# Optimization experiments

Measured on AMD Instinct MI355X. Metric: run time of the kernel, lower is better.

## Reference

```python
import jax, jax.numpy as jnp
import numpy as np

VOCAB = 32000
EMB = 256
DEC = 1024
ENC = 1024  # 2 * encoder hidden (bi-directional)
B = 128
S = 512


def setup_inputs() -> dict:
    key = jax.random.key(0)
    ks = jax.random.split(key, 16)
    s = 0.02
    return {
        "inputs": jax.random.randint(ks[0], (B, 1), 0, VOCAB),
        "decoder_hidden": jax.random.normal(ks[1], (B, DEC), jnp.float32),
        "encoder_output": jax.random.normal(ks[2], (B, S, ENC), jnp.float32),
        "emb": jax.random.normal(ks[3], (VOCAB, EMB), jnp.float32) * s,
        "W1": jax.random.normal(ks[4], (ENC, DEC), jnp.float32) * s,
        "b1": jnp.zeros((DEC,), jnp.float32),
        "W2": jax.random.normal(ks[5], (DEC, DEC), jnp.float32) * s,
        "b2": jnp.zeros((DEC,), jnp.float32),
        "Wv": jax.random.normal(ks[6], (DEC, 1), jnp.float32) * s,
        "bv": jnp.zeros((1,), jnp.float32),
        "lstm_k": jax.random.normal(ks[7], (ENC + EMB, 4 * DEC), jnp.float32) * s,
        "lstm_rk": jax.random.normal(ks[8], (DEC, 4 * DEC), jnp.float32) * s,
        "lstm_b": jnp.zeros((4 * DEC,), jnp.float32),
        "fc_W": jax.random.normal(ks[9], (DEC, VOCAB), jnp.float32) * s,
        "fc_b": jnp.zeros((VOCAB,), jnp.float32),
    }


def reference(inputs, decoder_hidden, encoder_output, emb, W1, b1, W2, b2,
              Wv, bv, lstm_k, lstm_rk, lstm_b, fc_W, fc_b):
    # Bahdanau additive attention
    # score: (B, S, 1)
    hidden_proj = decoder_hidden @ W2 + b2                      # (B, DEC)
    score = jnp.tanh(encoder_output @ W1 + b1 + hidden_proj[:, None, :]) @ Wv + bv
    attention_weights = jax.nn.softmax(score, axis=1)           # (B, S, 1)
    context = jnp.sum(attention_weights * encoder_output, axis=1)  # (B, ENC)

    # embedding lookup of the single input token, concat [context, embed]
    x = jnp.concatenate([context, emb[inputs[:, 0]]], axis=-1)  # (B, ENC+EMB)

    # single-step LSTM. Original calls rnn(inputs) with NO initial_state,
    # so h0 = c0 = 0 and the recurrent kernel contributes nothing this step.
    z = x @ lstm_k + lstm_b + jnp.zeros((B, DEC), x.dtype) @ lstm_rk  # (B, 4*DEC)
    i, f, g, o = jnp.split(z, 4, axis=-1)  # keras gate order i,f,c,o
    c = jax.nn.sigmoid(f) * 0.0 + jax.nn.sigmoid(i) * jnp.tanh(g)
    h = jax.nn.sigmoid(o) * jnp.tanh(c)

    logits = h @ fc_W + fc_b                                    # (B, VOCAB)
    return logits, (h, c), attention_weights
```

## Files before the change

kernel.cpp:

```cpp
#include <hip/hip_runtime.h>
#include <hip/hip_bf16.h>

#define VOCAB 32000
#define EMB   256
#define DEC   1024
#define ENC   1024
#define BB    128
#define SS    512
#define MTOT  (BB * SS)
#define XCOLS (ENC + EMB)
#define NG    (4 * DEC)

typedef _Float16 half8  __attribute__((ext_vector_type(8)));
typedef _Float16 half4  __attribute__((ext_vector_type(4)));
typedef float    floatx4 __attribute__((ext_vector_type(4)));

__device__ __forceinline__ float fast_tanh(float x) {
    float e = __builtin_amdgcn_exp2f(x * 2.885390082f);
    return 1.0f - 2.0f * __builtin_amdgcn_rcpf(e + 1.0f);
}
__device__ __forceinline__ float fast_sigmoid(float x) {
    float e = __builtin_amdgcn_exp2f(-x * 1.442695041f);
    return __builtin_amdgcn_rcpf(1.0f + e);
}

__global__ void k_transpose_w1(const float* __restrict__ W1, _Float16* __restrict__ w1t) {
    __shared__ float tile[32][33];
    const int k0 = blockIdx.y * 32, n0 = blockIdx.x * 32;
    const int tx = threadIdx.x, ty = threadIdx.y;
    #pragma unroll
    for (int j = 0; j < 4; ++j)
        tile[ty + j * 8][tx] = W1[(size_t)(k0 + ty + j * 8) * DEC + n0 + tx];
    __syncthreads();
    #pragma unroll
    for (int j = 0; j < 4; ++j)
        w1t[(size_t)(n0 + ty + j * 8) * ENC + k0 + tx] = (_Float16)tile[tx][ty + j * 8];
}

__global__ void k_hidden_proj(const float* __restrict__ dh, const float* __restrict__ W2,
                              const float* __restrict__ b1, const float* __restrict__ b2,
                              float* __restrict__ hp) {
    __shared__ float xs[8 * 1024];
    const int t = threadIdx.x;
    const int n = blockIdx.x * 128 + t;
    const int b0 = blockIdx.y * 8;
    for (int i = t; i < 2048; i += 128)
        ((floatx4*)xs)[i] = ((const floatx4*)(dh + (size_t)b0 * 1024))[i];
    __syncthreads();
    float acc[8] = {0, 0, 0, 0, 0, 0, 0, 0};
    for (int k = 0; k < 1024; ++k) {
        float wval = W2[(size_t)k * 1024 + n];
        #pragma unroll
        for (int j = 0; j < 8; ++j) acc[j] += xs[j * 1024 + k] * wval;
    }
    const float bias = b1[n] + b2[n];
    #pragma unroll
    for (int j = 0; j < 8; ++j) hp[(size_t)(b0 + j) * 1024 + n] = acc[j] + bias;
}

__global__ __launch_bounds__(256) void k_score(
    const float* __restrict__ enc, const _Float16* __restrict__ w1t,
    const float* __restrict__ hp, const float* __restrict__ wv,
    float* __restrict__ scores)
{
    __shared__ _Float16 As[128 * 40];
    __shared__ _Float16 Bs[128 * 40];
    const int n0 = blockIdx.x * 128;
    const int m0 = blockIdx.y * 128;
    const int b  = m0 >> 9;
    const int t = threadIdx.x;
    const int lane = t & 63, w = t >> 6;
    const int wm = (w >> 1) * 64, wn = (w & 1) * 64;
    const int col = lane & 15, q = lane >> 4;

    floatx4 acc[4][4];
    #pragma unroll
    for (int i = 0; i < 4; ++i)
        #pragma unroll
        for (int j = 0; j < 4; ++j) acc[i][j] = (floatx4){0.f, 0.f, 0.f, 0.f};

    const int sr = t >> 1;
    const int sc = (t & 1) * 16;
    const float*    ag = enc + (size_t)(m0 + sr) * ENC + sc;
    const _Float16* bg = w1t + (size_t)(n0 + sr) * ENC + sc;
    _Float16* asw = &As[sr * 40 + sc];
    _Float16* bsw = &Bs[sr * 40 + sc];

    for (int k0 = 0; k0 < ENC; k0 += 32) {
        __syncthreads();
        floatx4 a0 = *(const floatx4*)(ag + k0);
        floatx4 a1 = *(const floatx4*)(ag + k0 + 4);
        floatx4 a2 = *(const floatx4*)(ag + k0 + 8);
        floatx4 a3 = *(const floatx4*)(ag + k0 + 12);
        half8 bv0 = *(const half8*)(bg + k0);
        half8 bv1 = *(const half8*)(bg + k0 + 8);
        half8 ha, hb;
        #pragma unroll
        for (int e = 0; e < 4; ++e) { ha[e] = (_Float16)a0[e]; ha[e + 4] = (_Float16)a1[e]; }
        #pragma unroll
        for (int e = 0; e < 4; ++e) { hb[e] = (_Float16)a2[e]; hb[e + 4] = (_Float16)a3[e]; }
        *(half8*)(asw)     = ha;
        *(half8*)(asw + 8) = hb;
        *(half8*)(bsw)     = bv0;
        *(half8*)(bsw + 8) = bv1;
        __syncthreads();
        half8 af[4], bf[4];
        #pragma unroll
        for (int i = 0; i < 4; ++i)
            af[i] = *(const half8*)(&As[(wm + i * 16 + col) * 40 + q * 8]);
        #pragma unroll
        for (int j = 0; j < 4; ++j)
            bf[j] = *(const half8*)(&Bs[(wn + j * 16 + col) * 40 + q * 8]);
        #pragma unroll
        for (int i = 0; i < 4; ++i)
            #pragma unroll
            for (int j = 0; j < 4; ++j)
                acc[i][j] = __builtin_amdgcn_mfma_f32_16x16x32_f16(af[i], bf[j], acc[i][j], 0, 0, 0);
    }

    float hpv[4], wvv[4];
    #pragma unroll
    for (int j = 0; j < 4; ++j) {
        int n = n0 + wn + j * 16 + col;
        hpv[j] = hp[b * 1024 + n];
        wvv[j] = wv[n];
    }
    #pragma unroll
    for (int i = 0; i < 4; ++i) {
        float rs0 = 0.f, rs1 = 0.f, rs2 = 0.f, rs3 = 0.f;
        #pragma unroll
        for (int j = 0; j < 4; ++j) {
            rs0 += fast_tanh(acc[i][j][0] + hpv[j]) * wvv[j];
            rs1 += fast_tanh(acc[i][j][1] + hpv[j]) * wvv[j];
            rs2 += fast_tanh(acc[i][j][2] + hpv[j]) * wvv[j];
            rs3 += fast_tanh(acc[i][j][3] + hpv[j]) * wvv[j];
        }
        #pragma unroll
        for (int off = 1; off < 16; off <<= 1) {
            rs0 += __shfl_xor(rs0, off);
            rs1 += __shfl_xor(rs1, off);
            rs2 += __shfl_xor(rs2, off);
            rs3 += __shfl_xor(rs3, off);
        }
        if (col == 0) {
            const int mrow = m0 + wm + i * 16 + q * 4;
            atomicAdd(&scores[mrow + 0], rs0);
            atomicAdd(&scores[mrow + 1], rs1);
            atomicAdd(&scores[mrow + 2], rs2);
            atomicAdd(&scores[mrow + 3], rs3);
        }
    }
}

__global__ void k_softmax_emb(const float* __restrict__ scores, const int* __restrict__ tok,
                              const float* __restrict__ emb, float* __restrict__ aw,
                              float* __restrict__ x) {
    const int b = blockIdx.x, t = threadIdx.x;
    float s0 = scores[b * SS + t];
    float s1 = scores[b * SS + 256 + t];
    float mx = fmaxf(s0, s1);
    for (int off = 32; off; off >>= 1) mx = fmaxf(mx, __shfl_xor(mx, off));
    __shared__ float redm[4], reds[4];
    const int w = t >> 6, lane = t & 63;
    if (lane == 0) redm[w] = mx;
    __syncthreads();
    mx = fmaxf(fmaxf(redm[0], redm[1]), fmaxf(redm[2], redm[3]));
    float e0 = exp2f((s0 - mx) * 1.44269504f);
    float e1 = exp2f((s1 - mx) * 1.44269504f);
    float sm = e0 + e1;
    for (int off = 32; off; off >>= 1) sm += __shfl_xor(sm, off);
    if (lane == 0) reds[w] = sm;
    __syncthreads();
    sm = reds[0] + reds[1] + reds[2] + reds[3];
    const float inv = 1.0f / sm;
    aw[b * SS + t]       = e0 * inv;
    aw[b * SS + 256 + t] = e1 * inv;
    x[(size_t)b * XCOLS + ENC + t] = emb[(size_t)tok[b] * EMB + t];
}

__global__ void k_context(const float* __restrict__ enc, const float* __restrict__ aw,
                          float* __restrict__ x) {
    const int b = blockIdx.x >> 2;
    const int e = (blockIdx.x & 3) * 256 + threadIdx.x;
    const float* ep = enc + (size_t)b * SS * ENC + e;
    const float* ap = aw + b * SS;
    float acc = 0.f;
    #pragma unroll 8
    for (int s = 0; s < SS; ++s) acc += ap[s] * ep[(size_t)s * ENC];
    x[(size_t)b * XCOLS + e] = acc;
}

__global__ void k_lstm(const float* __restrict__ x, const float* __restrict__ lk,
                       float* __restrict__ z) {
    __shared__ float xs[8 * XCOLS];
    const int t = threadIdx.x;
    const int n = blockIdx.x * 128 + t;
    const int b0 = blockIdx.y * 8;
    for (int i = t; i < 2560; i += 128)
        ((floatx4*)xs)[i] = ((const floatx4*)(x + (size_t)b0 * XCOLS))[i];
    __syncthreads();
    float acc[8] = {0, 0, 0, 0, 0, 0, 0, 0};
    for (int k = 0; k < XCOLS; ++k) {
        float wval = lk[(size_t)k * NG + n];
        #pragma unroll
        for (int j = 0; j < 8; ++j) acc[j] += xs[j * XCOLS + k] * wval;
    }
    #pragma unroll
    for (int j = 0; j < 8; ++j) z[(size_t)(b0 + j) * NG + n] = acc[j];
}

__global__ void k_gates(const float* __restrict__ z, const float* __restrict__ lb,
                        float* __restrict__ h_out, float* __restrict__ c_out) {
    const int idx = blockIdx.x * 256 + threadIdx.x;
    const int b = idx >> 10, d = idx & 1023;
    const float* zb = z + (size_t)b * NG;
    float iv = zb[d]        + lb[d];
    float gv = zb[d + 2048] + lb[d + 2048];
    float ov = zb[d + 3072] + lb[d + 3072];
    float c = fast_sigmoid(iv) * fast_tanh(gv);
    float h = fast_sigmoid(ov) * fast_tanh(c);
    h_out[idx] = h;
    c_out[idx] = c;
}

__global__ __launch_bounds__(256) void k_fc(
    const float* __restrict__ hsrc, const float* __restrict__ fcW,
    const float* __restrict__ fcb, float* __restrict__ logits)
{
    __shared__ _Float16 As[128 * 40];
    __shared__ _Float16 Bs[128 * 40];
    const int n0 = blockIdx.x * 128;
    const int t = threadIdx.x;
    const int lane = t & 63, w = t >> 6;
    const int wm = (w >> 1) * 64, wn = (w & 1) * 64;
    const int col = lane & 15, q = lane >> 4;

    floatx4 acc[4][4];
    #pragma unroll
    for (int i = 0; i < 4; ++i)
        #pragma unroll
        for (int j = 0; j < 4; ++j) acc[i][j] = (floatx4){0.f, 0.f, 0.f, 0.f};

    const int sr = t >> 1, sc = (t & 1) * 16;
    const float* ag = hsrc + (size_t)sr * 1024 + sc;
    _Float16* asw = &As[sr * 40 + sc];
    const int bn = (t & 31) * 4;
    const int bk = (t >> 5) * 4;

    for (int k0 = 0; k0 < 1024; k0 += 32) {
        __syncthreads();
        floatx4 a0 = *(const floatx4*)(ag + k0);
        floatx4 a1 = *(const floatx4*)(ag + k0 + 4);
        floatx4 a2 = *(const floatx4*)(ag + k0 + 8);
        floatx4 a3 = *(const floatx4*)(ag + k0 + 12);
        half8 ha, hb;
        #pragma unroll
        for (int e = 0; e < 4; ++e) { ha[e] = (_Float16)a0[e]; ha[e + 4] = (_Float16)a1[e]; }
        #pragma unroll
        for (int e = 0; e < 4; ++e) { hb[e] = (_Float16)a2[e]; hb[e + 4] = (_Float16)a3[e]; }
        *(half8*)(asw)     = ha;
        *(half8*)(asw + 8) = hb;
        floatx4 w0 = *(const floatx4*)(fcW + (size_t)(k0 + bk + 0) * VOCAB + n0 + bn);
        floatx4 w1 = *(const floatx4*)(fcW + (size_t)(k0 + bk + 1) * VOCAB + n0 + bn);
        floatx4 w2 = *(const floatx4*)(fcW + (size_t)(k0 + bk + 2) * VOCAB + n0 + bn);
        floatx4 w3 = *(const floatx4*)(fcW + (size_t)(k0 + bk + 3) * VOCAB + n0 + bn);
        #pragma unroll
        for (int c = 0; c < 4; ++c) {
            half4 p = { (_Float16)w0[c], (_Float16)w1[c], (_Float16)w2[c], (_Float16)w3[c] };
            *(half4*)(&Bs[(bn + c) * 40 + bk]) = p;
        }
        __syncthreads();
        half8 af[4], bf[4];
        #pragma unroll
        for (int i = 0; i < 4; ++i)
            af[i] = *(const half8*)(&As[(wm + i * 16 + col) * 40 + q * 8]);
        #pragma unroll
        for (int j = 0; j < 4; ++j)
            bf[j] = *(const half8*)(&Bs[(wn + j * 16 + col) * 40 + q * 8]);
        #pragma unroll
        for (int i = 0; i < 4; ++i)
            #pragma unroll
            for (int j = 0; j < 4; ++j)
                acc[i][j] = __builtin_amdgcn_mfma_f32_16x16x32_f16(af[i], bf[j], acc[i][j], 0, 0, 0);
    }

    float fcbv[4];
    #pragma unroll
    for (int j = 0; j < 4; ++j) fcbv[j] = fcb[n0 + wn + j * 16 + col];
    #pragma unroll
    for (int i = 0; i < 4; ++i)
        #pragma unroll
        for (int j = 0; j < 4; ++j)
            #pragma unroll
            for (int r = 0; r < 4; ++r) {
                const int row = wm + i * 16 + q * 4 + r;
                logits[(size_t)row * VOCAB + n0 + wn + j * 16 + col] = acc[i][j][r] + fcbv[j];
            }
}

extern "C" void kernel_launch(void* const* d_in, const int* in_sizes, int n_in,
                              void* d_out, int out_size, void* d_ws, size_t ws_size,
                              hipStream_t stream) {
    const int*   tok    = (const int*)d_in[0];
    const float* dh     = (const float*)d_in[1];
    const float* enc    = (const float*)d_in[2];
    const float* emb    = (const float*)d_in[3];
    const float* W1     = (const float*)d_in[4];
    const float* b1     = (const float*)d_in[5];
    const float* W2     = (const float*)d_in[6];
    const float* b2     = (const float*)d_in[7];
    const float* Wv     = (const float*)d_in[8];
    const float* lstm_k = (const float*)d_in[10];
    const float* lstm_b = (const float*)d_in[12];
    const float* fc_W   = (const float*)d_in[13];
    const float* fc_b   = (const float*)d_in[14];

    float* out    = (float*)d_out;
    float* logits = out;
    float* h_out  = out + 4096000;
    float* c_out  = out + 4096000 + 131072;
    float* aw     = out + 4096000 + 262144;

    char* ws = (char*)d_ws;
    _Float16* w1t    = (_Float16*)ws;
    float*    hp     = (float*)(ws + 2097152);
    float*    scores = (float*)(ws + 2621440);
    float*    x      = (float*)(ws + 2883584);
    float*    z      = (float*)(ws + 3538944);

    hipMemsetAsync(scores, 0, MTOT * sizeof(float), stream);
    k_transpose_w1<<<dim3(32, 32), dim3(32, 8), 0, stream>>>(W1, w1t);
    k_hidden_proj<<<dim3(8, 16), 128, 0, stream>>>(dh, W2, b1, b2, hp);
    k_score<<<dim3(8, 512), 256, 0, stream>>>(enc, w1t, hp, Wv, scores);
    k_softmax_emb<<<128, 256, 0, stream>>>(scores, tok, emb, aw, x);
    k_context<<<512, 256, 0, stream>>>(enc, aw, x);
    k_lstm<<<dim3(32, 16), 128, 0, stream>>>(x, lstm_k, z);
    k_gates<<<512, 256, 0, stream>>>(z, lstm_b, h_out, c_out);
    k_fc<<<250, 256, 0, stream>>>(h_out, fc_W, fc_b, logits);
}
```

Measured before the change: 984.2 us.

## Fuse LSTM gates, split context over sequence, remap score tiles, re-grid hidden proj

Several independent changes. The LSTM matmul is fused with the gate nonlinearities and computes only the i, g and o columns, skipping the dead f gate and the z buffer. The context reduction is split across 16 sequence chunks with vectorized loads and combined by atomic adds into a zeroed x buffer. The score GEMM block index is remapped so consecutive blocks on one XCD share the same M rows, and hidden_proj is re-gridded to one batch row per block. The exchange is atomic traffic in context, and LSTM/hidden-proj kernels that now re-read the weights once per batch row (128 times) instead of once per 8 rows.

Result: slower. 1.058 ms (+7.5%).

```diff
diff --git a/kernel.cpp b/kernel.cpp
--- a/kernel.cpp
+++ b/kernel.cpp
@@ -40,22 +40,16 @@
 __global__ void k_hidden_proj(const float* __restrict__ dh, const float* __restrict__ W2,
                               const float* __restrict__ b1, const float* __restrict__ b2,
                               float* __restrict__ hp) {
-    __shared__ float xs[8 * 1024];
-    const int t = threadIdx.x;
-    const int n = blockIdx.x * 128 + t;
-    const int b0 = blockIdx.y * 8;
-    for (int i = t; i < 2048; i += 128)
-        ((floatx4*)xs)[i] = ((const floatx4*)(dh + (size_t)b0 * 1024))[i];
-    __syncthreads();
-    float acc[8] = {0, 0, 0, 0, 0, 0, 0, 0};
-    for (int k = 0; k < 1024; ++k) {
-        float wval = W2[(size_t)k * 1024 + n];
-        #pragma unroll
-        for (int j = 0; j < 8; ++j) acc[j] += xs[j * 1024 + k] * wval;
-    }
-    const float bias = b1[n] + b2[n];
-    #pragma unroll
-    for (int j = 0; j < 8; ++j) hp[(size_t)(b0 + j) * 1024 + n] = acc[j] + bias;
+    __shared__ float xs[1024];
+    const int b = blockIdx.x;
+    const int n = blockIdx.y * 256 + threadIdx.x;
+    if (threadIdx.x < 256)
+        ((floatx4*)xs)[threadIdx.x] = ((const floatx4*)(dh + (size_t)b * 1024))[threadIdx.x];
+    __syncthreads();
+    float acc = b1[n] + b2[n];
+    #pragma unroll 8
+    for (int k = 0; k < 1024; ++k) acc += xs[k] * W2[(size_t)k * 1024 + n];
+    hp[(size_t)b * 1024 + n] = acc;
 }
 
 __global__ __launch_bounds__(256) void k_score(
@@ -65,8 +59,11 @@
 {
     __shared__ _Float16 As[128 * 40];
     __shared__ _Float16 Bs[128 * 40];
-    const int n0 = blockIdx.x * 128;
-    const int m0 = blockIdx.y * 128;
+    const int L = blockIdx.y * 8 + blockIdx.x;
+    const int xcd = L & 7;
+    const int s8  = L >> 3;
+    const int m0 = (xcd * 64 + (s8 >> 3)) * 128;
+    const int n0 = (s8 & 7) * 128;
     const int b  = m0 >> 9;
     const int t = threadIdx.x;
     const int lane = t & 63, w = t >> 6;
@@ -180,47 +177,52 @@
 
 __global__ void k_context(const float* __restrict__ enc, const float* __restrict__ aw,
                           float* __restrict__ x) {
-    const int b = blockIdx.x >> 2;
-    const int e = (blockIdx.x & 3) * 256 + threadIdx.x;
-    const float* ep = enc + (size_t)b * SS * ENC + e;
-    const float* ap = aw + b * SS;
-    float acc = 0.f;
-    #pragma unroll 8
-    for (int s = 0; s < SS; ++s) acc += ap[s] * ep[(size_t)s * ENC];
-    x[(size_t)b * XCOLS + e] = acc;
-}
-
-__global__ void k_lstm(const float* __restrict__ x, const float* __restrict__ lk,
-                       float* __restrict__ z) {
-    __shared__ float xs[8 * XCOLS];
-    const int t = threadIdx.x;
-    const int n = blockIdx.x * 128 + t;
-    const int b0 = blockIdx.y * 8;
-    for (int i = t; i < 2560; i += 128)
-        ((floatx4*)xs)[i] = ((const floatx4*)(x + (size_t)b0 * XCOLS))[i];
-    __syncthreads();
-    float acc[8] = {0, 0, 0, 0, 0, 0, 0, 0};
+    const int b = blockIdx.x;
+    const int s0 = blockIdx.y * 32;
+    const int e4 = threadIdx.x;
+    const float* ep = enc + (size_t)(b * SS + s0) * ENC;
+    const float* ap = aw + b * SS + s0;
+    floatx4 acc = {0.f, 0.f, 0.f, 0.f};
+    #pragma unroll
+    for (int s = 0; s < 32; ++s) {
+        const float wv = ap[s];
+        const floatx4 v = ((const floatx4*)(ep + (size_t)s * ENC))[e4];
+        acc[0] += wv * v[0]; acc[1] += wv * v[1];
+        acc[2] += wv * v[2]; acc[3] += wv * v[3];
+    }
+    float* xp = x + (size_t)b * XCOLS + 4 * e4;
+    atomicAdd(xp + 0, acc[0]);
+    atomicAdd(xp + 1, acc[1]);
+    atomicAdd(xp + 2, acc[2]);
+    atomicAdd(xp + 3, acc[3]);
+}
+
+__global__ void k_lstm_fused(const float* __restrict__ x, const float* __restrict__ lk,
+                             const float* __restrict__ lb,
+                             float* __restrict__ h_out, float* __restrict__ c_out) {
+    __shared__ float xs[XCOLS];
+    const int b = blockIdx.x;
+    const int n = blockIdx.y * 256 + threadIdx.x;
+    for (int i = threadIdx.x; i < XCOLS / 4; i += 256)
+        ((floatx4*)xs)[i] = ((const floatx4*)(x + (size_t)b * XCOLS))[i];
+    __syncthreads();
+    const float* ki = lk + n;
+    const float* kg = lk + 2048 + n;
+    const float* ko = lk + 3072 + n;
+    float ai = 0.f, ag = 0.f, ao = 0.f;
+    #pragma unroll 4
     for (int k = 0; k < XCOLS; ++k) {
-        float wval = lk[(size_t)k * NG + n];
-        #pragma unroll
-        for (int j = 0; j < 8; ++j) acc[j] += xs[j * XCOLS + k] * wval;
-    }
-    #pragma unroll
-    for (int j = 0; j < 8; ++j) z[(size_t)(b0 + j) * NG + n] = acc[j];
-}
-
-__global__ void k_gates(const float* __restrict__ z, const float* __restrict__ lb,
-                        float* __restrict__ h_out, float* __restrict__ c_out) {
-    const int idx = blockIdx.x * 256 + threadIdx.x;
-    const int b = idx >> 10, d = idx & 1023;
-    const float* zb = z + (size_t)b * NG;
-    float iv = zb[d]        + lb[d];
-    float gv = zb[d + 2048] + lb[d + 2048];
-    float ov = zb[d + 3072] + lb[d + 3072];
-    float c = fast_sigmoid(iv) * fast_tanh(gv);
-    float h = fast_sigmoid(ov) * fast_tanh(c);
-    h_out[idx] = h;
-    c_out[idx] = c;
+        const float xv = xs[k];
+        const size_t off = (size_t)k * NG;
+        ai += xv * ki[off];
+        ag += xv * kg[off];
+        ao += xv * ko[off];
+    }
+    ai += lb[n]; ag += lb[2048 + n]; ao += lb[3072 + n];
+    const float c = fast_sigmoid(ai) * fast_tanh(ag);
+    const float h = fast_sigmoid(ao) * fast_tanh(c);
+    h_out[b * 1024 + n] = h;
+    c_out[b * 1024 + n] = c;
 }
 
 __global__ __launch_bounds__(256) void k_fc(
@@ -326,15 +328,13 @@
     float*    hp     = (float*)(ws + 2097152);
     float*    scores = (float*)(ws + 2621440);
     float*    x      = (float*)(ws + 2883584);
-    float*    z      = (float*)(ws + 3538944);
-
-    hipMemsetAsync(scores, 0, MTOT * sizeof(float), stream);
+
+    hipMemsetAsync(scores, 0, 262144 + 655360, stream);
     k_transpose_w1<<<dim3(32, 32), dim3(32, 8), 0, stream>>>(W1, w1t);
-    k_hidden_proj<<<dim3(8, 16), 128, 0, stream>>>(dh, W2, b1, b2, hp);
+    k_hidden_proj<<<dim3(128, 4), 256, 0, stream>>>(dh, W2, b1, b2, hp);
     k_score<<<dim3(8, 512), 256, 0, stream>>>(enc, w1t, hp, Wv, scores);
     k_softmax_emb<<<128, 256, 0, stream>>>(scores, tok, emb, aw, x);
-    k_context<<<512, 256, 0, stream>>>(enc, aw, x);
-    k_lstm<<<dim3(32, 16), 128, 0, stream>>>(x, lstm_k, z);
-    k_gates<<<512, 256, 0, stream>>>(z, lstm_b, h_out, c_out);
+    k_context<<<dim3(128, 16), 256, 0, stream>>>(enc, aw, x);
+    k_lstm_fused<<<dim3(128, 4), 256, 0, stream>>>(x, lstm_k, lstm_b, h_out, c_out);
     k_fc<<<250, 256, 0, stream>>>(h_out, fc_W, fc_b, logits);
 }
```
